# Optimization experiments

Hardware: AMD Instinct MI355X
Metric: run time of the kernel (lower is better)

Reference implementation:

```python
import jax, jax.numpy as jnp
import numpy as np

B, N, Z, E, K = 2, 64, 128, 64, 64


def setup_inputs() -> dict:
    key = jax.random.key(0)
    ks = jax.random.split(key, 8)
    emb1 = jax.random.normal(ks[0], (B, N, Z), dtype=jnp.float32)
    ef = jax.random.normal(ks[1], (B, N, N, E), dtype=jnp.float32)
    Wz = jax.random.normal(ks[2], (3, Z, K), dtype=jnp.float32) / np.float32(np.sqrt(Z))
    bz = jnp.zeros((3, K), dtype=jnp.float32)
    Wef = jax.random.normal(ks[3], (3, E, K), dtype=jnp.float32) / np.float32(np.sqrt(E))
    # pattern embedding: 6 rows, padding_idx=0 -> row 0 is zeros
    table = jax.random.normal(ks[4], (6, K), dtype=jnp.float32).at[0].set(0.0)
    Wm = jax.random.normal(ks[5], (2, K, K), dtype=jnp.float32) / np.float32(np.sqrt(K))
    bm = jnp.zeros((2, K), dtype=jnp.float32)
    return {"emb1": emb1, "ef": ef, "Wz": Wz, "bz": bz, "Wef": Wef,
            "table": table, "Wm": Wm, "bm": bm}


def _tuple_pattern(n):
    # start at 1, diag(i,i,i)=2, (i,:,i)=3, (:,j,j)=4, (i,i,:)=5
    idx = jnp.arange(n)
    tp = jnp.ones((n, n, n), dtype=jnp.int32)
    tp = tp.at[idx, idx, idx].set(2)
    tp = tp.at[idx, :, idx].set(3)
    tp = tp.at[:, idx, idx].set(4)
    tp = tp.at[idx, idx, :].set(5)
    return tp


def reference(emb1, ef, Wz, bz, Wef, table, Wm, bm):
    # z_lins: Dense(Z->K) with SiLU activation
    z0 = jax.nn.silu(emb1 @ Wz[0] + bz[0])  # (B,N,K)
    z1 = jax.nn.silu(emb1 @ Wz[1] + bz[1])
    z2 = jax.nn.silu(emb1 @ Wz[2] + bz[2])
    # ef_lins: Dense(E->K), no bias, no activation
    e0 = ef @ Wef[0]  # (B,N,N,K)
    e1 = ef @ Wef[1]
    e2 = ef @ Wef[2]
    # 3-way outer broadcasts -> (B,N,N,N,K)
    z_mixed = z0[:, None, None, :, :] * z1[:, :, None, None, :] * z2[:, None, :, None, :]
    ef_mixed = e0[:, None, :, :, :] * e1[:, :, None, :, :] * e2[:, :, :, None, :]
    n = emb1.shape[1]
    pat = table[_tuple_pattern(n)]  # (N,N,N,K)
    x = z_mixed * ef_mixed * pat[None]  # (B,N,N,N,K)
    # Residual(mlp_num=2): two Dense(K->K, SiLU) layers + skip
    h = jax.nn.silu(x @ Wm[0] + bm[0])
    h = jax.nn.silu(h @ Wm[1] + bm[1])
    return h + x
```

## Files before the change

### kernel.cpp

```cpp
#include <hip/hip_runtime.h>

typedef __attribute__((ext_vector_type(4))) float f4;
typedef __attribute__((ext_vector_type(8))) short bf8;
typedef __attribute__((ext_vector_type(4))) float f32x4;
typedef __attribute__((ext_vector_type(2))) unsigned int u32x2;
typedef __attribute__((ext_vector_type(4))) unsigned int u32x4;

__device__ __forceinline__ float silu_f(float v) {
    return v * __builtin_amdgcn_rcpf(1.0f + __expf(-v));
}
__device__ __forceinline__ ushort f2bf(float f) {
    unsigned u = __float_as_uint(f);
    u += 0x7fff + ((u >> 16) & 1);
    return (ushort)(u >> 16);
}
__device__ __forceinline__ unsigned cvtpk(float lo, float hi) {
    unsigned r;
    asm("v_cvt_pk_bf16_f32 %0, %1, %2" : "=v"(r) : "v"(lo), "v"(hi));
    return r;
}
__device__ __forceinline__ void cvt8(u32x4 v, f4& lo, f4& hi) {
    lo[0] = __uint_as_float(v[0] << 16);
    lo[1] = __uint_as_float(v[0] & 0xffff0000u);
    lo[2] = __uint_as_float(v[1] << 16);
    lo[3] = __uint_as_float(v[1] & 0xffff0000u);
    hi[0] = __uint_as_float(v[2] << 16);
    hi[1] = __uint_as_float(v[2] & 0xffff0000u);
    hi[2] = __uint_as_float(v[3] << 16);
    hi[3] = __uint_as_float(v[3] & 0xffff0000u);
}

extern "C" __global__ void k_zw(const float* __restrict__ emb1,
                                const float* __restrict__ Wz,
                                const float* __restrict__ bz,
                                const float* __restrict__ Wm,
                                float* __restrict__ z,
                                ushort* __restrict__ WT) {
    if (blockIdx.x < 96) {
        int tid = blockIdx.x * 256 + threadIdx.x;
        int k = tid & 63;
        int n = (tid >> 6) & 63;
        int b = (tid >> 12) & 1;
        int l = tid >> 13;
        const float* er = emb1 + (b * 64 + n) * 128;
        const float* w  = Wz + l * 8192 + k;
        float acc = bz[l * 64 + k];
        #pragma unroll 8
        for (int c = 0; c < 128; ++c) acc = fmaf(er[c], w[c * 64], acc);
        z[tid] = silu_f(acc);
    } else {
        int tid = (blockIdx.x - 96) * 256 + threadIdx.x;
        int l = tid >> 12, n = (tid >> 6) & 63, k = tid & 63;
        WT[tid] = f2bf(Wm[l * 4096 + k * 64 + n]);
    }
}

extern "C" __global__ void k_e(const float* __restrict__ ef,
                               const float* __restrict__ Wef,
                               const float* __restrict__ z,
                               ushort* __restrict__ e) {
    int tid = blockIdx.x * 256 + threadIdx.x;
    int k0  = (tid & 15) * 4;
    int row = (tid >> 4) & 8191;
    int l   = tid >> 17;
    const float* efr = ef + row * 64;
    const float* w   = Wef + l * 4096 + k0;
    f4 acc = {0.f, 0.f, 0.f, 0.f};
    #pragma unroll
    for (int c4 = 0; c4 < 16; ++c4) {
        f4 ev = *(const f4*)(efr + c4 * 4);
        #pragma unroll
        for (int q = 0; q < 4; ++q)
            acc += ev[q] * *(const f4*)(w + (c4 * 4 + q) * 64);
    }
    int b  = row >> 12;
    int mn = (l == 1) ? ((row >> 6) & 63) : (row & 63);
    acc *= *(const f4*)(z + l * 8192 + b * 4096 + mn * 64 + k0);
    u32x2 pk = {cvtpk(acc[0], acc[1]), cvtpk(acc[2], acc[3])};
    *(u32x2*)(e + l * 524288 + row * 64 + k0) = pk;
}

extern "C" __global__ void __launch_bounds__(256, 4)
k_main(const ushort* __restrict__ e, const float* __restrict__ table,
       const ushort* __restrict__ WT, const float* __restrict__ bm,
       float* __restrict__ out) {
    __shared__ ushort Wl[8192];
    __shared__ ushort XH[8192];

    const int t   = threadIdx.x;
    const int raw = blockIdx.x;
    const int sem = (raw & 7) * 256 + (raw >> 3);
    const int ig  = sem >> 8;
    const int pos = sem & 255;
    const int b   = pos >> 7;
    const int jq  = (pos >> 3) & 15;
    const int i   = ig * 8 + (pos & 7);
    const int j0  = jq * 4;

    #pragma unroll
    for (int p = 0; p < 4; ++p) {
        int g   = p * 256 + t;
        int row = g >> 3;
        int cb  = (g & 7) * 16;
        u32x4 v = *(const u32x4*)(WT + g * 8);
        *(u32x4*)((char*)Wl + row * 128 + (cb ^ ((row & 7) << 4))) = v;
    }

    const int r  = t >> 2;
    const int c0 = (t & 3) << 4;
    const int ln = t & 63, w = t >> 6;
    const int lr = ln & 15, lg = ln >> 4;
    const int abyte = (w * 16 + lr) * 128;
    const int arx   = (lr & 7) << 4;
    const int orr = ln >> 3, os = ln & 7;
    const int obrow = ((lr & 8) ? (8192 + w * 2048) : (w * 2048)) + (lr & 7) * 256;

    const ushort* e1p = e + 524288 + ((b * 64 + i) * 64 + r) * 64 + c0;
    u32x4 e1r0 = *(const u32x4*)(e1p);
    u32x4 e1r1 = *(const u32x4*)(e1p + 8);
    f4 pe1t[4];
    {
        f4 a, bq, c, d;
        cvt8(e1r0, a, bq); cvt8(e1r1, c, d);
        pe1t[0] = a  * *(const f4*)(table + 64 + c0);
        pe1t[1] = bq * *(const f4*)(table + 64 + c0 + 4);
        pe1t[2] = c  * *(const f4*)(table + 64 + c0 + 8);
        pe1t[3] = d  * *(const f4*)(table + 64 + c0 + 12);
    }

    const ushort* e0base = e + ((b * 64 + j0) * 64 + r) * 64 + c0;
    const ushort* e2base = e + 1048576 + ((b * 64 + i) * 64 + j0) * 64 + c0;
    float* ob = out + (size_t)((b * 64 + i) * 64 + j0) * 4096;

    u32x4 ce0a = *(const u32x4*)(e0base);
    u32x4 ce0b = *(const u32x4*)(e0base + 8);

    __syncthreads();

    #pragma unroll 1
    for (int jt = 0; jt < 4; ++jt) {
        const int jj = j0 + jt;

        {
            const ushort* e2p = e2base + jt * 64;
            u32x4 e2a = *(const u32x4*)(e2p);
            u32x4 e2b = *(const u32x4*)(e2p + 8);
            f4 e0f[4], e2f[4];
            cvt8(ce0a, e0f[0], e0f[1]); cvt8(ce0b, e0f[2], e0f[3]);
            cvt8(e2a,  e2f[0], e2f[1]); cvt8(e2b,  e2f[2], e2f[3]);
            f4 xv[4];
            bool slow = (i == jj) || (r == jj) || (r == i);
            if (slow) {
                int p = (i == jj) ? 5 : (jj == r) ? 4 : 3;
                const float* pp = table + p * 64 + c0;
                f4 e1f[4];
                cvt8(e1r0, e1f[0], e1f[1]); cvt8(e1r1, e1f[2], e1f[3]);
                #pragma unroll
                for (int q = 0; q < 4; ++q)
                    xv[q] = e1f[q] * *(const f4*)(pp + 4 * q) * e2f[q] * e0f[q];
            } else {
                #pragma unroll
                for (int q = 0; q < 4; ++q)
                    xv[q] = pe1t[q] * e2f[q] * e0f[q];
            }
            unsigned xw[8];
            #pragma unroll
            for (int q = 0; q < 4; ++q) {
                xw[2 * q]     = cvtpk(xv[q][0], xv[q][1]);
                xw[2 * q + 1] = cvtpk(xv[q][2], xv[q][3]);
            }
            char* rowp = (char*)XH + r * 128;
            const int rx = (r & 7) << 4;
            u32x4 vlo = {xw[0], xw[1], xw[2], xw[3]};
            u32x4 vhi = {xw[4], xw[5], xw[6], xw[7]};
            *(u32x4*)(rowp + ((c0 * 2)      ^ rx)) = vlo;
            *(u32x4*)(rowp + ((c0 * 2 + 16) ^ rx)) = vhi;
        }

        if (jt < 3) {
            const ushort* ne0 = e0base + (jt + 1) * 4096;
            ce0a = *(const u32x4*)(ne0);
            ce0b = *(const u32x4*)(ne0 + 8);
        }

        bf8 a0 = *(const bf8*)((const char*)XH + abyte + ((     lg * 16) ^ arx));
        bf8 a1 = *(const bf8*)((const char*)XH + abyte + ((64 + lg * 16) ^ arx));
        #pragma unroll
        for (int nt = 0; nt < 4; ++nt) {
            const char* wb = (const char*)Wl + (nt * 16 + lr) * 128;
            bf8 b0 = *(const bf8*)(wb + ((     lg * 16) ^ arx));
            bf8 b1 = *(const bf8*)(wb + ((64 + lg * 16) ^ arx));
            f32x4 acc = *(const f4*)(bm + nt * 16 + lg * 4);
            acc = __builtin_amdgcn_mfma_f32_16x16x32_bf16(b0, a0, acc, 0, 0, 0);
            acc = __builtin_amdgcn_mfma_f32_16x16x32_bf16(b1, a1, acc, 0, 0, 0);
            unsigned pk0 = cvtpk(silu_f(acc[0]), silu_f(acc[1]));
            unsigned pk1 = cvtpk(silu_f(acc[2]), silu_f(acc[3]));
            u32x2 hv = {pk0, pk1};
            *(u32x2*)((char*)XH + 8192 + abyte + ((nt * 32 + lg * 8) ^ arx)) = hv;
        }

        bf8 h0 = *(const bf8*)((const char*)XH + 8192 + abyte + ((     lg * 16) ^ arx));
        bf8 h1 = *(const bf8*)((const char*)XH + 8192 + abyte + ((64 + lg * 16) ^ arx));
        u32x2 rrv[4];
        #pragma unroll
        for (int nt = 0; nt < 4; ++nt)
            rrv[nt] = *(const u32x2*)((const char*)XH + abyte +
                                      ((nt * 32 + lg * 8) ^ arx));
        #pragma unroll
        for (int nt = 0; nt < 4; ++nt) {
            const char* wb = (const char*)Wl + (64 + nt * 16 + lr) * 128;
            bf8 b0 = *(const bf8*)(wb + ((     lg * 16) ^ arx));
            bf8 b1 = *(const bf8*)(wb + ((64 + lg * 16) ^ arx));
            f32x4 acc = *(const f4*)(bm + 64 + nt * 16 + lg * 4);
            acc = __builtin_amdgcn_mfma_f32_16x16x32_bf16(b0, h0, acc, 0, 0, 0);
            acc = __builtin_amdgcn_mfma_f32_16x16x32_bf16(b1, h1, acc, 0, 0, 0);
            f4 ov;
            ov[0] = silu_f(acc[0]) + __uint_as_float(rrv[nt][0] << 16);
            ov[1] = silu_f(acc[1]) + __uint_as_float(rrv[nt][0] & 0xffff0000u);
            ov[2] = silu_f(acc[2]) + __uint_as_float(rrv[nt][1] << 16);
            ov[3] = silu_f(acc[3]) + __uint_as_float(rrv[nt][1] & 0xffff0000u);
            *(f4*)((char*)XH + obrow + ((nt * 64 + lg * 16) ^ ((lr & 7) << 4))) = ov;
        }

        float* obj = ob + (size_t)jt * 4096 + w * 16 * 64;
        #pragma unroll
        for (int v = 0; v < 4; ++v) {
            const int rw = (v & 1) * 8 + orr;
            const int rbase = ((v & 1) ? (8192 + w * 2048) : (w * 2048))
                            + (rw & 7) * 256;
            f4 val = *(const f4*)((const char*)XH + rbase +
                     ((((v >> 1) * 128) + os * 16) ^ ((rw & 7) << 4)));
            *(f4*)(obj + rw * 64 + (v >> 1) * 32 + os * 4) = val;
        }
    }
}

extern "C" void kernel_launch(void* const* d_in, const int* in_sizes, int n_in,
                              void* d_out, int out_size, void* d_ws, size_t ws_size,
                              hipStream_t stream) {
    const float* emb1  = (const float*)d_in[0];
    const float* ef    = (const float*)d_in[1];
    const float* Wz    = (const float*)d_in[2];
    const float* bz    = (const float*)d_in[3];
    const float* Wef   = (const float*)d_in[4];
    const float* table = (const float*)d_in[5];
    const float* Wm    = (const float*)d_in[6];
    const float* bm    = (const float*)d_in[7];
    float* out = (float*)d_out;

    float*  zbuf = (float*)d_ws;
    ushort* ebuf = (ushort*)(zbuf + 24576);
    ushort* WT   = ebuf + 1572864;

    k_zw  <<<128,  256, 0, stream>>>(emb1, Wz, bz, Wm, zbuf, WT);
    k_e   <<<1536, 256, 0, stream>>>(ef, Wef, zbuf, ebuf);
    k_main<<<2048, 256, 0, stream>>>(ebuf, table, WT, bm, out);
}
```

Measured before the change: 59.40 us.

## Compute ef projections with bf16 MFMA using pretransposed Wef

The ef @ Wef projection kernel switches from scalar fp32 FMAs, where each thread computes four outputs over 64 inputs, to bf16 MFMA 16x16x32 instructions. Each 64-thread block stages 16 ef rows into swizzled LDS and multiplies them against a bf16-transposed Wef prepared in the setup kernel. This reduces the ALU work in the e-projection stage. In exchange, ef is rounded to bf16 before the matmul, which costs some accuracy, and the setup kernel launches extra blocks.

```diff
diff --git a/kernel.cpp b/kernel.cpp
--- a/kernel.cpp
+++ b/kernel.cpp
@@ -34,8 +34,10 @@
                                 const float* __restrict__ Wz,
                                 const float* __restrict__ bz,
                                 const float* __restrict__ Wm,
+                                const float* __restrict__ Wef,
                                 float* __restrict__ z,
-                                ushort* __restrict__ WT) {
+                                ushort* __restrict__ WT,
+                                ushort* __restrict__ WefT) {
     if (blockIdx.x < 96) {
         int tid = blockIdx.x * 256 + threadIdx.x;
         int k = tid & 63;
@@ -48,36 +50,74 @@
         #pragma unroll 8
         for (int c = 0; c < 128; ++c) acc = fmaf(er[c], w[c * 64], acc);
         z[tid] = silu_f(acc);
-    } else {
+    } else if (blockIdx.x < 128) {
         int tid = (blockIdx.x - 96) * 256 + threadIdx.x;
         int l = tid >> 12, n = (tid >> 6) & 63, k = tid & 63;
         WT[tid] = f2bf(Wm[l * 4096 + k * 64 + n]);
-    }
-}
-
-extern "C" __global__ void k_e(const float* __restrict__ ef,
-                               const float* __restrict__ Wef,
-                               const float* __restrict__ z,
-                               ushort* __restrict__ e) {
-    int tid = blockIdx.x * 256 + threadIdx.x;
-    int k0  = (tid & 15) * 4;
-    int row = (tid >> 4) & 8191;
-    int l   = tid >> 17;
-    const float* efr = ef + row * 64;
-    const float* w   = Wef + l * 4096 + k0;
-    f4 acc = {0.f, 0.f, 0.f, 0.f};
+    } else {
+        int tid = (blockIdx.x - 128) * 256 + threadIdx.x;
+        int l = tid >> 12, n = (tid >> 6) & 63, k = tid & 63;
+        WefT[tid] = f2bf(Wef[l * 4096 + k * 64 + n]);
+    }
+}
+
+extern "C" __global__ void __launch_bounds__(64)
+k_e(const float* __restrict__ ef, const ushort* __restrict__ WefT,
+    const float* __restrict__ z, ushort* __restrict__ e) {
+    __shared__ ushort EF[2048];
+
+    const int t   = threadIdx.x;
+    const int blk = blockIdx.x;
+    const int l    = blk >> 9;
+    const int rt16 = blk & 511;
+    const int r0g  = rt16 * 16;
+
+    const int rl = t >> 2;
+    const int c0 = (t & 3) << 4;
+    {
+        const float* src = ef + (size_t)(r0g + rl) * 64 + c0;
+        unsigned xw[8];
+        #pragma unroll
+        for (int q = 0; q < 4; ++q) {
+            f4 v = *(const f4*)(src + 4 * q);
+            xw[2 * q]     = cvtpk(v[0], v[1]);
+            xw[2 * q + 1] = cvtpk(v[2], v[3]);
+        }
+        char* rowp = (char*)EF + rl * 128;
+        const int rx = (rl & 7) << 4;
+        u32x4 vlo = {xw[0], xw[1], xw[2], xw[3]};
+        u32x4 vhi = {xw[4], xw[5], xw[6], xw[7]};
+        *(u32x4*)(rowp + ((c0 * 2)      ^ rx)) = vlo;
+        *(u32x4*)(rowp + ((c0 * 2 + 16) ^ rx)) = vhi;
+    }
+
+    const int lr = t & 15, lg = t >> 4;
+    const int abyte = lr * 128;
+    const int arx   = (lr & 7) << 4;
+    bf8 a0 = *(const bf8*)((const char*)EF + abyte + ((     lg * 16) ^ arx));
+    bf8 a1 = *(const bf8*)((const char*)EF + abyte + ((64 + lg * 16) ^ arx));
+
+    const int b  = r0g >> 12;
+    const int fi = (r0g >> 6) & 63;
+    const int se = (r0g & 63) + lr;
+    const int mn = (l == 1) ? fi : se;
+    const float* zb = z + l * 8192 + b * 4096 + mn * 64;
+    ushort* erow = e + (size_t)l * 524288 + (size_t)(r0g + lr) * 64;
+
     #pragma unroll
-    for (int c4 = 0; c4 < 16; ++c4) {
-        f4 ev = *(const f4*)(efr + c4 * 4);
-        #pragma unroll
-        for (int q = 0; q < 4; ++q)
-            acc += ev[q] * *(const f4*)(w + (c4 * 4 + q) * 64);
-    }
-    int b  = row >> 12;
-    int mn = (l == 1) ? ((row >> 6) & 63) : (row & 63);
-    acc *= *(const f4*)(z + l * 8192 + b * 4096 + mn * 64 + k0);
-    u32x2 pk = {cvtpk(acc[0], acc[1]), cvtpk(acc[2], acc[3])};
-    *(u32x2*)(e + l * 524288 + row * 64 + k0) = pk;
+    for (int nt = 0; nt < 4; ++nt) {
+        const ushort* wp = WefT + l * 4096 + (nt * 16 + lr) * 64 + lg * 8;
+        bf8 b0 = *(const bf8*)(wp);
+        bf8 b1 = *(const bf8*)(wp + 32);
+        f32x4 acc = {0.f, 0.f, 0.f, 0.f};
+        acc = __builtin_amdgcn_mfma_f32_16x16x32_bf16(b0, a0, acc, 0, 0, 0);
+        acc = __builtin_amdgcn_mfma_f32_16x16x32_bf16(b1, a1, acc, 0, 0, 0);
+        const int k0 = nt * 16 + lg * 4;
+        f4 zf = *(const f4*)(zb + k0);
+        u32x2 pk = {cvtpk(acc[0] * zf[0], acc[1] * zf[1]),
+                    cvtpk(acc[2] * zf[2], acc[3] * zf[3])};
+        *(u32x2*)(erow + k0) = pk;
+    }
 }
 
 extern "C" __global__ void __launch_bounds__(256, 4)
@@ -251,8 +291,9 @@
     float*  zbuf = (float*)d_ws;
     ushort* ebuf = (ushort*)(zbuf + 24576);
     ushort* WT   = ebuf + 1572864;
-
-    k_zw  <<<128,  256, 0, stream>>>(emb1, Wz, bz, Wm, zbuf, WT);
-    k_e   <<<1536, 256, 0, stream>>>(ef, Wef, zbuf, ebuf);
+    ushort* WefT = WT + 8192;
+
+    k_zw  <<<176,  256, 0, stream>>>(emb1, Wz, bz, Wm, Wef, zbuf, WT, WefT);
+    k_e   <<<1536, 64,  0, stream>>>(ef, WefT, zbuf, ebuf);
     k_main<<<2048, 256, 0, stream>>>(ebuf, table, WT, bm, out);
 }
```

Measured after the change: 49.54 us. -16.6%, faster.
